# Optimization experiments

Measured on AMD Instinct MI355X. Metric: run time of the kernel, lower is better.

The kernel has to match this reference:

```python
import jax, jax.numpy as jnp
import numpy as np

DIM = 384
HEADS = 6
HEAD_DIM = DIM // HEADS
MLP_DIM = int(DIM * 4.0)
EPS = 1e-5


def layer_norm(x, g, b):
    mu = jnp.mean(x, axis=-1, keepdims=True)
    var = jnp.mean(jnp.square(x - mu), axis=-1, keepdims=True)
    return (x - mu) * jax.lax.rsqrt(var + EPS) * g + b


def setup_inputs() -> dict:
    key = jax.random.key(0)
    ks = jax.random.split(key, 12)
    s = 0.02
    return {
        "x": jax.random.normal(ks[0], (8, 2048, DIM), dtype=jnp.float32),
        "ln1_g": jnp.ones((DIM,), jnp.float32),
        "ln1_b": jnp.zeros((DIM,), jnp.float32),
        "qkv_w": jax.random.normal(ks[1], (DIM, 3 * DIM), jnp.float32) * s,
        "qkv_b": jnp.zeros((3 * DIM,), jnp.float32),
        "proj_w": jax.random.normal(ks[2], (DIM, DIM), jnp.float32) * s,
        "proj_b": jnp.zeros((DIM,), jnp.float32),
        "ln2_g": jnp.ones((DIM,), jnp.float32),
        "ln2_b": jnp.zeros((DIM,), jnp.float32),
        "fc1_w": jax.random.normal(ks[3], (DIM, MLP_DIM), jnp.float32) * s,
        "fc1_b": jnp.zeros((MLP_DIM,), jnp.float32),
        "fc2_w": jax.random.normal(ks[4], (MLP_DIM, DIM), jnp.float32) * s,
        "fc2_b": jnp.zeros((DIM,), jnp.float32),
    }


def reference(x, ln1_g, ln1_b, qkv_w, qkv_b, proj_w, proj_b,
              ln2_g, ln2_b, fc1_w, fc1_b, fc2_w, fc2_b):
    B, N, C = x.shape
    # --- attention ---
    h = layer_norm(x, ln1_g, ln1_b)
    qkv = h @ qkv_w + qkv_b  # [B,N,3C]
    qkv = qkv.reshape(B, N, 3, HEADS, HEAD_DIM)
    q, k, v = jnp.moveaxis(qkv, 2, 0)  # each [B,N,H,D]
    scale = HEAD_DIM ** -0.5
    attn = jnp.einsum('bnhd,bmhd->bhnm', q, k) * scale  # [B,H,N,N]
    attn = jax.nn.softmax(attn, axis=-1)
    o = jnp.einsum('bhnm,bmhd->bnhd', attn, v).reshape(B, N, C)
    x = x + o @ proj_w + proj_b
    # --- mlp ---
    h = layer_norm(x, ln2_g, ln2_b)
    h = jax.nn.gelu(h @ fc1_w + fc1_b, approximate=False)
    x = x + h @ fc2_w + fc2_b
    return x
```

## Files before the change

### kernel.cpp

```cpp
#include <hip/hip_runtime.h>
#include <hip/hip_bf16.h>

#define DIM   384
#define SEQ   2048
#define BATCH 8
#define NHEAD 6
#define HD    64
#define MLPD  1536
#define MTOT  (BATCH*SEQ)

typedef __attribute__((ext_vector_type(8))) short bf16x8;
typedef __attribute__((ext_vector_type(4))) float f32x4;

static __device__ __forceinline__ float bf2f(unsigned short u){
    union { float f; unsigned int i; } v; v.i = ((unsigned int)u) << 16; return v.f;
}
static __device__ __forceinline__ unsigned short f2bf(float f){
    union { float f; unsigned int i; } v; v.f = f;
    unsigned int r = v.i + 0x7fffu + ((v.i >> 16) & 1u);
    return (unsigned short)(r >> 16);
}
static __device__ __forceinline__ unsigned int asu(float f){
    union { float f; unsigned int i; } v; v.f = f; return v.i;
}
static __device__ __forceinline__ void gload_lds16(const unsigned short* g, unsigned short* l){
    __builtin_amdgcn_global_load_lds(
        (__attribute__((address_space(1))) void*)(g),
        (__attribute__((address_space(3))) void*)(l), 16, 0, 0);
}
static __device__ __forceinline__ void barx(){
    asm volatile("" ::: "memory");
    __builtin_amdgcn_s_barrier();
    asm volatile("" ::: "memory");
}
#define WAITVM(N) asm volatile("s_waitcnt vmcnt(" #N ")" ::: "memory")

static __device__ __forceinline__ int xcd_lin(){
    return (blockIdx.x & 7) * ((int)gridDim.x >> 3) + ((int)blockIdx.x >> 3);
}

__global__ __launch_bounds__(256) void wt_all_kernel(
    const float* __restrict__ qkv_w, const float* __restrict__ proj_w,
    const float* __restrict__ fc1_w, const float* __restrict__ fc2_w,
    unsigned short* __restrict__ o_qkv, unsigned short* __restrict__ o_prj,
    unsigned short* __restrict__ o_fc1, unsigned short* __restrict__ o_fc2)
{
    __shared__ float tile[64][68];
    int bid = blockIdx.x;
    const float* W; unsigned short* Wt; int K, N, tk, tn;
    if (bid < 108)      { W = qkv_w; Wt = o_qkv; K = 384;  N = 1152; tk = bid/18;        tn = bid%18; }
    else if (bid < 144) { W = proj_w; Wt = o_prj; K = 384;  N = 384;  tk = (bid-108)/6;  tn = (bid-108)%6; }
    else if (bid < 288) { W = fc1_w; Wt = o_fc1; K = 384;  N = 1536; tk = (bid-144)/24; tn = (bid-144)%24; }
    else                { W = fc2_w; Wt = o_fc2; K = 1536; N = 384;  tk = (bid-288)/6;  tn = (bid-288)%6; }
    int t = threadIdx.x;
    int lr = t >> 4, lc = (t & 15) * 4;
#pragma unroll
    for (int p = 0; p < 4; p++){
        float4 v = *(const float4*)(W + (size_t)(tk*64 + p*16 + lr) * N + tn*64 + lc);
        *(float4*)&tile[p*16 + lr][lc] = v;
    }
    __syncthreads();
    int n = t >> 2, k0 = (t & 3) * 16;
    unsigned int w[8];
#pragma unroll
    for (int i = 0; i < 8; i++)
        w[i] = (unsigned int)f2bf(tile[k0 + 2*i][n]) | ((unsigned int)f2bf(tile[k0 + 2*i + 1][n]) << 16);
    unsigned short* dst = Wt + (size_t)(tn*64 + n) * K + tk*64 + k0;
    *(uint4*)(dst)     = make_uint4(w[0], w[1], w[2], w[3]);
    *(uint4*)(dst + 8) = make_uint4(w[4], w[5], w[6], w[7]);
}

__global__ __launch_bounds__(256) void ln_kernel(const float* __restrict__ x,
                                                 const float* __restrict__ g,
                                                 const float* __restrict__ b,
                                                 unsigned short* __restrict__ out){
    int row  = blockIdx.x * 4 + (threadIdx.x >> 6);
    int lane = threadIdx.x & 63;
    const float* xr = x + (size_t)row * DIM;
    float v[6];
#pragma unroll
    for (int p = 0; p < 3; p++){
        float2 t = *(const float2*)(xr + lane * 2 + p * 128);
        v[2*p] = t.x; v[2*p+1] = t.y;
    }
    float s = 0.f, sq = 0.f;
#pragma unroll
    for (int i = 0; i < 6; i++){ s += v[i]; sq += v[i] * v[i]; }
#pragma unroll
    for (int off = 1; off < 64; off <<= 1){
        s  += __shfl_xor(s, off);
        sq += __shfl_xor(sq, off);
    }
    float mu   = s * (1.0f / DIM);
    float var  = sq * (1.0f / DIM) - mu * mu;
    float rstd = rsqrtf(var + 1e-5f);
    unsigned short* orow = out + (size_t)row * DIM;
#pragma unroll
    for (int p = 0; p < 3; p++){
        int c = lane * 2 + p * 128;
        float h0 = (v[2*p]   - mu) * rstd * g[c]   + b[c];
        float h1 = (v[2*p+1] - mu) * rstd * g[c+1] + b[c+1];
        unsigned int pk = (unsigned int)f2bf(h0) | ((unsigned int)f2bf(h1) << 16);
        *(unsigned int*)(orow + c) = pk;
    }
}

template<int EPI, int NC>
__global__ __launch_bounds__(128, 3) void gemm_kernel(
    const unsigned short* __restrict__ A, const unsigned short* __restrict__ Bt,
    const float* __restrict__ bias, int K, int N,
    const float* __restrict__ resid, float* __restrict__ outf,
    unsigned short* __restrict__ outb,
    unsigned short* __restrict__ qb, unsigned short* __restrict__ kb2,
    unsigned short* __restrict__ vb)
{
    __shared__ __align__(16) unsigned short smem[64*64 + 128*64];
    unsigned short* As = smem;
    unsigned short* Bs = smem + 64*64;
    int t = threadIdx.x;
    int wid = t >> 6, lane = t & 63, quad = lane >> 4, l15 = lane & 15;
    int lin = xcd_lin();
    int row0 = (lin / NC) * 64, col0 = (lin % NC) * 128;
    int sr = lane >> 3, sc = lane & 7;
    int scl = (sc ^ sr) * 8;

    const unsigned short* Ab = A  + (size_t)row0 * K;
    const unsigned short* Bb = Bt + (size_t)col0 * K;

    f32x4 acc[2][8];
    f32x4 zz = {0.f, 0.f, 0.f, 0.f};
#pragma unroll
    for (int i = 0; i < 2; i++)
#pragma unroll
        for (int j = 0; j < 8; j++) acc[i][j] = zz;

    for (int k0 = 0; k0 < K; k0 += 64){
        __syncthreads();
#pragma unroll
        for (int jj = 0; jj < 4; jj++){
            int rb = wid * 32 + jj * 8;
            gload_lds16(Ab + (size_t)(rb + sr) * K + k0 + scl, &As[rb * 64]);
        }
#pragma unroll
        for (int jj = 0; jj < 8; jj++){
            int rb = wid * 64 + jj * 8;
            gload_lds16(Bb + (size_t)(rb + sr) * K + k0 + scl, &Bs[rb * 64]);
        }
        __syncthreads();
#pragma unroll
        for (int kk = 0; kk < 2; kk++){
            bf16x8 af[2], bf[8];
#pragma unroll
            for (int i = 0; i < 2; i++){
                int r = wid*32 + i*16 + l15;
                af[i] = *(const bf16x8*)&As[r * 64 + (((kk*4 + quad) ^ (l15 & 7)) * 8)];
            }
#pragma unroll
            for (int j = 0; j < 8; j++){
                int r = j*16 + l15;
                bf[j] = *(const bf16x8*)&Bs[r * 64 + (((kk*4 + quad) ^ (l15 & 7)) * 8)];
            }
#pragma unroll
            for (int i = 0; i < 2; i++)
#pragma unroll
                for (int j = 0; j < 8; j++)
                    acc[i][j] = __builtin_amdgcn_mfma_f32_16x16x32_bf16(af[i], bf[j], acc[i][j], 0, 0, 0);
        }
    }

    if (EPI == 0 && col0 >= 768){
        __syncthreads();
        unsigned short* T = smem;
#pragma unroll
        for (int i = 0; i < 2; i++)
#pragma unroll
            for (int j = 0; j < 8; j++){
                int gcl = j*16 + l15;
                float bia = bias[col0 + gcl];
                int nsl0 = wid*32 + i*16 + quad*4;
#pragma unroll
                for (int r = 0; r < 4; r++)
                    T[gcl * 72 + nsl0 + r] = f2bf(acc[i][j][r] + bia);
            }
        __syncthreads();
        int rem = (col0 - 768) + t;
        int head = rem >> 6, d = rem & 63;
        int bidx = row0 >> 11, ns0 = row0 & 2047;
        unsigned short* dst = vb + ((size_t)((bidx * NHEAD + head) * 64 + d)) * SEQ + ns0;
        const unsigned short* src = T + t * 72;
#pragma unroll
        for (int m = 0; m < 8; m++)
            *(uint4*)(dst + m*8) = *(const uint4*)(src + m*8);
        return;
    }

#pragma unroll
    for (int i = 0; i < 2; i++){
#pragma unroll
        for (int j = 0; j < 8; j++){
            int gr0 = row0 + wid*32 + i*16 + quad*4;
            int gc  = col0 + j*16 + l15;
            float bia = bias[gc];
#pragma unroll
            for (int r = 0; r < 4; r++){
                int gr = gr0 + r;
                float val = acc[i][j][r] + bia;
                if (EPI == 1){
                    outf[(size_t)gr * N + gc] = resid[(size_t)gr * N + gc] + val;
                } else if (EPI == 2){
                    float u = val * (1.0f + 0.044715f * val * val);
                    float e = __builtin_amdgcn_exp2f(u * 2.3025851f);
                    outb[(size_t)gr * N + gc] = f2bf(val * e / (e + 1.0f));
                } else {
                    int trip = gc / 384, remq = gc - trip * 384;
                    int head = remq >> 6, d = remq & 63;
                    int bidx = gr >> 11, ns = gr & 2047;
                    size_t off = ((size_t)(bidx * NHEAD + head) * SEQ + ns) * 64 + d;
                    unsigned short* dstp = (trip == 0) ? qb : kb2;
                    dstp[off] = f2bf(val);
                }
            }
        }
    }
}

template<int LOFF>
static __device__ __forceinline__ void attn_tile(
    const bf16x8 (&qf)[2][2], const bf16x8& ones,
    const unsigned short* const (&kf_ptr)[4][2],
    const unsigned short* const (&vf_ptr)[2][4],
    const unsigned short* const (&pf_ptr)[2][2],
    uint2* const (&pw_ptr)[2][4],
    f32x4 (&sacc)[2], f32x4 (&oacc)[2][4])
{
    const f32x4 zz = {0.f, 0.f, 0.f, 0.f};
    f32x4 st[2][4];
#pragma unroll
    for (int n = 0; n < 4; n++){
        bf16x8 kf0 = *(const bf16x8*)(kf_ptr[n][0] + LOFF);
        bf16x8 kf1 = *(const bf16x8*)(kf_ptr[n][1] + LOFF);
#pragma unroll
        for (int h = 0; h < 2; h++){
            f32x4 z = __builtin_amdgcn_mfma_f32_16x16x32_bf16(kf0, qf[h][0], zz, 0, 0, 0);
            st[h][n] = __builtin_amdgcn_mfma_f32_16x16x32_bf16(kf1, qf[h][1], z, 0, 0, 0);
        }
    }
#pragma unroll
    for (int h = 0; h < 2; h++){
#pragma unroll
        for (int n = 0; n < 4; n++){
            float p0 = __builtin_amdgcn_exp2f(st[h][n][0]);
            float p1 = __builtin_amdgcn_exp2f(st[h][n][1]);
            float p2 = __builtin_amdgcn_exp2f(st[h][n][2]);
            float p3 = __builtin_amdgcn_exp2f(st[h][n][3]);
            unsigned int w0 = __builtin_amdgcn_perm(asu(p1), asu(p0), 0x07060302u);
            unsigned int w1 = __builtin_amdgcn_perm(asu(p3), asu(p2), 0x07060302u);
            *pw_ptr[h][n] = make_uint2(w0, w1);
        }
    }
    asm volatile("s_waitcnt lgkmcnt(0)" ::: "memory");
#pragma unroll
    for (int c = 0; c < 2; c++){
        bf16x8 pf[2];
#pragma unroll
        for (int h = 0; h < 2; h++)
            pf[h] = *(const bf16x8*)pf_ptr[c][h];
        sacc[0] = __builtin_amdgcn_mfma_f32_16x16x32_bf16(ones, pf[0], sacc[0], 0, 0, 0);
        sacc[1] = __builtin_amdgcn_mfma_f32_16x16x32_bf16(ones, pf[1], sacc[1], 0, 0, 0);
#pragma unroll
        for (int dn = 0; dn < 4; dn++){
            bf16x8 vf = *(const bf16x8*)(vf_ptr[c][dn] + LOFF);
            oacc[0][dn] = __builtin_amdgcn_mfma_f32_16x16x32_bf16(vf, pf[0], oacc[0][dn], 0, 0, 0);
            oacc[1][dn] = __builtin_amdgcn_mfma_f32_16x16x32_bf16(vf, pf[1], oacc[1][dn], 0, 0, 0);
        }
    }
}

__global__ __launch_bounds__(256, 3) void attn_kernel(const unsigned short* __restrict__ Q,
                                                      const unsigned short* __restrict__ Kb,
                                                      const unsigned short* __restrict__ Vt,
                                                      unsigned short* __restrict__ O){
    __shared__ __align__(16) unsigned short smem[16384 + 4*2048];

    int lin = xcd_lin();
    int qt = lin & 15, bh = lin >> 4;
    int t = threadIdx.x, wid = t >> 6, lane = t & 63, quad = lane >> 4, l15 = lane & 15;
    int l7 = l15 & 7;
    int q0 = qt * 128 + wid * 32;
    const unsigned short* Qp = Q  + (size_t)bh * SEQ * 64;
    const unsigned short* Kp = Kb + (size_t)bh * SEQ * 64;
    const unsigned short* Vp = Vt + (size_t)bh * 64 * SEQ;
    int sr = lane >> 3, sc = lane & 7;
    int scl = (sc ^ sr) * 8;

    const float QSCALE = 0.125f * 1.44269504f;
    bf16x8 qf[2][2];
#pragma unroll
    for (int h = 0; h < 2; h++){
#pragma unroll
        for (int c = 0; c < 2; c++){
            union { uint4 u; unsigned short s[8]; } cv;
            cv.u = *(const uint4*)(Qp + (size_t)(q0 + h*16 + l15) * 64 + c * 32 + quad * 8);
            bf16x8 f;
#pragma unroll
            for (int j = 0; j < 8; j++) f[j] = (short)f2bf(bf2f(cv.s[j]) * QSCALE);
            qf[h][c] = f;
        }
    }

    bf16x8 ones;
#pragma unroll
    for (int j = 0; j < 8; j++) ones[j] = (short)0x3F80;

    f32x4 oacc[2][4], sacc[2];
    f32x4 zz = {0.f, 0.f, 0.f, 0.f};
#pragma unroll
    for (int h = 0; h < 2; h++){
        sacc[h] = zz;
#pragma unroll
        for (int dn = 0; dn < 4; dn++) oacc[h][dn] = zz;
    }
    unsigned short* P = &smem[16384 + wid * 2048];

    const unsigned short* kf_ptr[4][2];
#pragma unroll
    for (int n = 0; n < 4; n++){
        int kv = n * 16 + l15;
        kf_ptr[n][0] = &smem[kv * 64 + ((quad       ^ (kv & 7)) * 8)];
        kf_ptr[n][1] = &smem[kv * 64 + (((4 + quad) ^ (kv & 7)) * 8)];
    }
    const unsigned short* vf_ptr[2][4];
#pragma unroll
    for (int c = 0; c < 2; c++)
#pragma unroll
        for (int dn = 0; dn < 4; dn++){
            int d = dn * 16 + l15;
            vf_ptr[c][dn] = &smem[4096 + d * 64 + (((c*4 + quad) ^ (d & 7)) * 8)];
        }
    const unsigned short* pf_ptr[2][2];
#pragma unroll
    for (int c = 0; c < 2; c++)
#pragma unroll
        for (int h = 0; h < 2; h++)
            pf_ptr[c][h] = P + (h*16 + l15) * 64 + (((c*4 + quad) ^ l7) * 8);
    uint2* pw_ptr[2][4];
#pragma unroll
    for (int h = 0; h < 2; h++)
#pragma unroll
        for (int n = 0; n < 4; n++){
            int qloc = h * 16 + l15;
            int chunk = n * 2 + (quad >> 1);
            pw_ptr[h][n] = (uint2*)(P + qloc * 64 + ((chunk ^ l7) * 8) + (quad & 1) * 4);
        }
    const unsigned short* kstage[2];
    const unsigned short* vstage[2];
    unsigned short* klds[2];
    unsigned short* vlds[2];
#pragma unroll
    for (int jj = 0; jj < 2; jj++){
        int rb = wid * 16 + jj * 8;
        kstage[jj] = Kp + (size_t)(rb + sr) * 64 + scl;
        vstage[jj] = Vp + (size_t)(rb + sr) * SEQ + scl;
        klds[jj] = &smem[rb * 64];
        vlds[jj] = &smem[4096 + rb * 64];
    }

#define AISSUE(BOFF) do { \
    _Pragma("unroll") \
    for (int jj = 0; jj < 2; jj++){ \
        gload_lds16(kstage[jj], klds[jj] + (BOFF)); \
        gload_lds16(vstage[jj], vlds[jj] + (BOFF)); \
        kstage[jj] += 64 * 64; \
        vstage[jj] += 64; \
    } } while(0)

    AISSUE(0);
    for (int p = 0; p < SEQ/128 - 1; p++){
        AISSUE(8192);
        WAITVM(4);
        barx();
        attn_tile<0>(qf, ones, kf_ptr, vf_ptr, pf_ptr, pw_ptr, sacc, oacc);
        barx();
        AISSUE(0);
        WAITVM(4);
        barx();
        attn_tile<8192>(qf, ones, kf_ptr, vf_ptr, pf_ptr, pw_ptr, sacc, oacc);
        barx();
    }
    AISSUE(8192);
    WAITVM(4);
    barx();
    attn_tile<0>(qf, ones, kf_ptr, vf_ptr, pf_ptr, pw_ptr, sacc, oacc);
    barx();
    WAITVM(0);
    barx();
    attn_tile<8192>(qf, ones, kf_ptr, vf_ptr, pf_ptr, pw_ptr, sacc, oacc);
#undef AISSUE

    int b = bh / NHEAD, hh = bh - b * NHEAD;
#pragma unroll
    for (int h = 0; h < 2; h++){
        float rd = 1.0f / sacc[h][0];
        size_t row = (size_t)(b * SEQ + q0 + h*16 + l15);
#pragma unroll
        for (int dn = 0; dn < 4; dn++){
            float v0 = oacc[h][dn][0] * rd, v1 = oacc[h][dn][1] * rd;
            float v2 = oacc[h][dn][2] * rd, v3 = oacc[h][dn][3] * rd;
            unsigned int w0 = (unsigned int)f2bf(v0) | ((unsigned int)f2bf(v1) << 16);
            unsigned int w1 = (unsigned int)f2bf(v2) | ((unsigned int)f2bf(v3) << 16);
            *(uint2*)(O + row * DIM + hh * 64 + dn * 16 + quad * 4) = make_uint2(w0, w1);
        }
    }
}

extern "C" void kernel_launch(void* const* d_in, const int* in_sizes, int n_in,
                              void* d_out, int out_size, void* d_ws, size_t ws_size,
                              hipStream_t stream){
    const float* x      = (const float*)d_in[0];
    const float* ln1_g  = (const float*)d_in[1];
    const float* ln1_b  = (const float*)d_in[2];
    const float* qkv_w  = (const float*)d_in[3];
    const float* qkv_b  = (const float*)d_in[4];
    const float* proj_w = (const float*)d_in[5];
    const float* proj_b = (const float*)d_in[6];
    const float* ln2_g  = (const float*)d_in[7];
    const float* ln2_b  = (const float*)d_in[8];
    const float* fc1_w  = (const float*)d_in[9];
    const float* fc1_b  = (const float*)d_in[10];
    const float* fc2_w  = (const float*)d_in[11];
    const float* fc2_b  = (const float*)d_in[12];
    float* out = (float*)d_out;

    char* p = (char*)d_ws;
    auto take = [&](size_t n){ char* r = p; p += (n + 255) & ~(size_t)255; return r; };
    unsigned short* wt_qkv = (unsigned short*)take((size_t)1152 * 384 * 2);
    unsigned short* wt_prj = (unsigned short*)take((size_t)384 * 384 * 2);
    unsigned short* wt_fc1 = (unsigned short*)take((size_t)1536 * 384 * 2);
    unsigned short* wt_fc2 = (unsigned short*)take((size_t)384 * 1536 * 2);
    unsigned short* rbig   = (unsigned short*)take((size_t)MTOT * 4 * DIM * 2);
    unsigned short* h2     = (unsigned short*)take((size_t)MTOT * DIM * 2);
    float*          x1     = (float*)take((size_t)MTOT * DIM * 4);

    unsigned short* h1     = rbig;
    unsigned short* qb     = rbig + (size_t)MTOT * DIM;
    unsigned short* kb     = qb   + (size_t)MTOT * DIM;
    unsigned short* vb     = kb   + (size_t)MTOT * DIM;
    unsigned short* attn_o = rbig;
    unsigned short* hm     = rbig;

    wt_all_kernel<<<dim3(432), 256, 0, stream>>>(qkv_w, proj_w, fc1_w, fc2_w,
                                                 wt_qkv, wt_prj, wt_fc1, wt_fc2);
    ln_kernel<<<dim3(MTOT/4), 256, 0, stream>>>(x, ln1_g, ln1_b, h1);
    gemm_kernel<0,9><<<dim3(2304), 128, 0, stream>>>(h1, wt_qkv, qkv_b, 384, 1152,
                                                     nullptr, nullptr, nullptr, qb, kb, vb);
    attn_kernel<<<dim3(768), 256, 0, stream>>>(qb, kb, vb, attn_o);
    gemm_kernel<1,3><<<dim3(768), 128, 0, stream>>>(attn_o, wt_prj, proj_b, 384, 384,
                                                    x, x1, nullptr, nullptr, nullptr, nullptr);
    ln_kernel<<<dim3(MTOT/4), 256, 0, stream>>>(x1, ln2_g, ln2_b, h2);
    gemm_kernel<2,12><<<dim3(3072), 128, 0, stream>>>(h2, wt_fc1, fc1_b, 384, 1536,
                                                      nullptr, nullptr, hm, nullptr, nullptr, nullptr);
    gemm_kernel<1,3><<<dim3(768), 128, 0, stream>>>(hm, wt_fc2, fc2_b, 1536, 384,
                                                    x1, out, nullptr, nullptr, nullptr, nullptr);
}
```

Measured before the change: 268.9 us.

## Enlarge GEMM tiles to 128x128 with 4 waves; add setprio around attention MFMAs

The GEMM kernel moves from 64x128 tiles with 2 waves to 128x128 tiles with 4 waves. Each wave still computes 32x128, and the B tile loaded into LDS is now shared by twice as many rows, which roughly halves B traffic per output. The V-transpose epilogue is split into two head halves so its staging buffer fits the new LDS layout, and grid sizes are halved to match. B fragments are now loaded and consumed one at a time, which lowers register pressure. Separately, the attention tile raises wave priority during its MFMA phases to help interleave with the exp work of other waves.

```diff
diff --git a/kernel.cpp b/kernel.cpp
--- a/kernel.cpp
+++ b/kernel.cpp
@@ -106,7 +106,7 @@
 }
 
 template<int EPI, int NC>
-__global__ __launch_bounds__(128, 3) void gemm_kernel(
+__global__ __launch_bounds__(256, 4) void gemm_kernel(
     const unsigned short* __restrict__ A, const unsigned short* __restrict__ Bt,
     const float* __restrict__ bias, int K, int N,
     const float* __restrict__ resid, float* __restrict__ outf,
@@ -114,13 +114,13 @@
     unsigned short* __restrict__ qb, unsigned short* __restrict__ kb2,
     unsigned short* __restrict__ vb)
 {
-    __shared__ __align__(16) unsigned short smem[64*64 + 128*64];
+    __shared__ __align__(16) unsigned short smem[2 * 8192];
     unsigned short* As = smem;
-    unsigned short* Bs = smem + 64*64;
+    unsigned short* Bs = smem + 8192;
     int t = threadIdx.x;
     int wid = t >> 6, lane = t & 63, quad = lane >> 4, l15 = lane & 15;
     int lin = xcd_lin();
-    int row0 = (lin / NC) * 64, col0 = (lin % NC) * 128;
+    int row0 = (lin / NC) * 128, col0 = (lin % NC) * 128;
     int sr = lane >> 3, sc = lane & 7;
     int scl = (sc ^ sr) * 8;
 
@@ -142,14 +142,14 @@
             gload_lds16(Ab + (size_t)(rb + sr) * K + k0 + scl, &As[rb * 64]);
         }
 #pragma unroll
-        for (int jj = 0; jj < 8; jj++){
-            int rb = wid * 64 + jj * 8;
+        for (int jj = 0; jj < 4; jj++){
+            int rb = wid * 32 + jj * 8;
             gload_lds16(Bb + (size_t)(rb + sr) * K + k0 + scl, &Bs[rb * 64]);
         }
         __syncthreads();
 #pragma unroll
         for (int kk = 0; kk < 2; kk++){
-            bf16x8 af[2], bf[8];
+            bf16x8 af[2];
 #pragma unroll
             for (int i = 0; i < 2; i++){
                 int r = wid*32 + i*16 + l15;
@@ -158,39 +158,40 @@
 #pragma unroll
             for (int j = 0; j < 8; j++){
                 int r = j*16 + l15;
-                bf[j] = *(const bf16x8*)&Bs[r * 64 + (((kk*4 + quad) ^ (l15 & 7)) * 8)];
+                bf16x8 bf = *(const bf16x8*)&Bs[r * 64 + (((kk*4 + quad) ^ (l15 & 7)) * 8)];
+                acc[0][j] = __builtin_amdgcn_mfma_f32_16x16x32_bf16(af[0], bf, acc[0][j], 0, 0, 0);
+                acc[1][j] = __builtin_amdgcn_mfma_f32_16x16x32_bf16(af[1], bf, acc[1][j], 0, 0, 0);
             }
+        }
+    }
+
+    if (EPI == 0 && col0 >= 768){
+        int bidx = row0 >> 11, ns0 = row0 & 2047;
+#pragma unroll
+        for (int half = 0; half < 2; half++){
+            __syncthreads();
+            unsigned short* T = smem;
 #pragma unroll
             for (int i = 0; i < 2; i++)
 #pragma unroll
-                for (int j = 0; j < 8; j++)
-                    acc[i][j] = __builtin_amdgcn_mfma_f32_16x16x32_bf16(af[i], bf[j], acc[i][j], 0, 0, 0);
-        }
-    }
-
-    if (EPI == 0 && col0 >= 768){
-        __syncthreads();
-        unsigned short* T = smem;
-#pragma unroll
-        for (int i = 0; i < 2; i++)
-#pragma unroll
-            for (int j = 0; j < 8; j++){
-                int gcl = j*16 + l15;
-                float bia = bias[col0 + gcl];
-                int nsl0 = wid*32 + i*16 + quad*4;
-#pragma unroll
-                for (int r = 0; r < 4; r++)
-                    T[gcl * 72 + nsl0 + r] = f2bf(acc[i][j][r] + bia);
-            }
-        __syncthreads();
-        int rem = (col0 - 768) + t;
-        int head = rem >> 6, d = rem & 63;
-        int bidx = row0 >> 11, ns0 = row0 & 2047;
-        unsigned short* dst = vb + ((size_t)((bidx * NHEAD + head) * 64 + d)) * SEQ + ns0;
-        const unsigned short* src = T + t * 72;
-#pragma unroll
-        for (int m = 0; m < 8; m++)
-            *(uint4*)(dst + m*8) = *(const uint4*)(src + m*8);
+                for (int jh = 0; jh < 4; jh++){
+                    int j = half*4 + jh;
+                    int d = jh*16 + l15;
+                    float bia = bias[col0 + half*64 + d];
+                    int nsl0 = wid*32 + i*16 + quad*4;
+#pragma unroll
+                    for (int r = 0; r < 4; r++)
+                        T[d * 136 + nsl0 + r] = f2bf(acc[i][j][r] + bia);
+                }
+            __syncthreads();
+            int head = ((col0 - 768) >> 6) + half;
+            int d = t >> 2, qq = t & 3;
+            unsigned short* dst = vb + ((size_t)((bidx * NHEAD + head) * 64 + d)) * SEQ + ns0 + qq*32;
+            const unsigned short* src = T + d * 136 + qq * 32;
+#pragma unroll
+            for (int m = 0; m < 4; m++)
+                *(uint4*)(dst + m*8) = *(const uint4*)(src + m*8);
+        }
         return;
     }
 
@@ -235,6 +236,7 @@
 {
     const f32x4 zz = {0.f, 0.f, 0.f, 0.f};
     f32x4 st[2][4];
+    __builtin_amdgcn_s_setprio(1);
 #pragma unroll
     for (int n = 0; n < 4; n++){
         bf16x8 kf0 = *(const bf16x8*)(kf_ptr[n][0] + LOFF);
@@ -245,6 +247,7 @@
             st[h][n] = __builtin_amdgcn_mfma_f32_16x16x32_bf16(kf1, qf[h][1], z, 0, 0, 0);
         }
     }
+    __builtin_amdgcn_s_setprio(0);
 #pragma unroll
     for (int h = 0; h < 2; h++){
 #pragma unroll
@@ -259,6 +262,7 @@
         }
     }
     asm volatile("s_waitcnt lgkmcnt(0)" ::: "memory");
+    __builtin_amdgcn_s_setprio(1);
 #pragma unroll
     for (int c = 0; c < 2; c++){
         bf16x8 pf[2];
@@ -274,6 +278,7 @@
             oacc[1][dn] = __builtin_amdgcn_mfma_f32_16x16x32_bf16(vf, pf[1], oacc[1][dn], 0, 0, 0);
         }
     }
+    __builtin_amdgcn_s_setprio(0);
 }
 
 __global__ __launch_bounds__(256, 3) void attn_kernel(const unsigned short* __restrict__ Q,
@@ -451,14 +456,14 @@
     wt_all_kernel<<<dim3(432), 256, 0, stream>>>(qkv_w, proj_w, fc1_w, fc2_w,
                                                  wt_qkv, wt_prj, wt_fc1, wt_fc2);
     ln_kernel<<<dim3(MTOT/4), 256, 0, stream>>>(x, ln1_g, ln1_b, h1);
-    gemm_kernel<0,9><<<dim3(2304), 128, 0, stream>>>(h1, wt_qkv, qkv_b, 384, 1152,
+    gemm_kernel<0,9><<<dim3(1152), 256, 0, stream>>>(h1, wt_qkv, qkv_b, 384, 1152,
                                                      nullptr, nullptr, nullptr, qb, kb, vb);
     attn_kernel<<<dim3(768), 256, 0, stream>>>(qb, kb, vb, attn_o);
-    gemm_kernel<1,3><<<dim3(768), 128, 0, stream>>>(attn_o, wt_prj, proj_b, 384, 384,
+    gemm_kernel<1,3><<<dim3(384), 256, 0, stream>>>(attn_o, wt_prj, proj_b, 384, 384,
                                                     x, x1, nullptr, nullptr, nullptr, nullptr);
     ln_kernel<<<dim3(MTOT/4), 256, 0, stream>>>(x1, ln2_g, ln2_b, h2);
-    gemm_kernel<2,12><<<dim3(3072), 128, 0, stream>>>(h2, wt_fc1, fc1_b, 384, 1536,
+    gemm_kernel<2,12><<<dim3(1536), 256, 0, stream>>>(h2, wt_fc1, fc1_b, 384, 1536,
                                                       nullptr, nullptr, hm, nullptr, nullptr, nullptr);
-    gemm_kernel<1,3><<<dim3(768), 128, 0, stream>>>(hm, wt_fc2, fc2_b, 1536, 384,
+    gemm_kernel<1,3><<<dim3(384), 256, 0, stream>>>(hm, wt_fc2, fc2_b, 1536, 384,
                                                     x1, out, nullptr, nullptr, nullptr, nullptr);
 }
```

After: 288.4 us. 7.3% more time.

## Add 32-row GEMM kernel for N=384 residual GEMMs and prioritize attention MFMA phases

Applied to the files above, without the earlier changes.

Adds a dedicated gemm32_kernel with 32x128 output tiles, used for the proj and fc2 GEMMs, whose output width of 384 left only 768 blocks with the old tile. The smaller row tile doubles the grid to 1536 blocks to fill more CUs, at the cost of more reloads of the B operand per output. The residual epilogue is removed from the generic GEMM. Separately, the attention tile raises wave priority with s_setprio around its MFMA phases, so that waves doing matrix work are favoured over those doing exp and LDS writes.

```diff
diff --git a/kernel.cpp b/kernel.cpp
--- a/kernel.cpp
+++ b/kernel.cpp
@@ -205,9 +205,7 @@
             for (int r = 0; r < 4; r++){
                 int gr = gr0 + r;
                 float val = acc[i][j][r] + bia;
-                if (EPI == 1){
-                    outf[(size_t)gr * N + gc] = resid[(size_t)gr * N + gc] + val;
-                } else if (EPI == 2){
+                if (EPI == 2){
                     float u = val * (1.0f + 0.044715f * val * val);
                     float e = __builtin_amdgcn_exp2f(u * 2.3025851f);
                     outb[(size_t)gr * N + gc] = f2bf(val * e / (e + 1.0f));
@@ -224,6 +222,82 @@
     }
 }
 
+template<int K>
+__global__ __launch_bounds__(128, 3) void gemm32_kernel(
+    const unsigned short* __restrict__ A, const unsigned short* __restrict__ Bt,
+    const float* __restrict__ bias, int N,
+    const float* __restrict__ resid, float* __restrict__ outf)
+{
+    __shared__ __align__(16) unsigned short smem[32*64 + 128*64];
+    unsigned short* As = smem;
+    unsigned short* Bs = smem + 32*64;
+    int t = threadIdx.x;
+    int wid = t >> 6, lane = t & 63, quad = lane >> 4, l15 = lane & 15;
+    int lin = xcd_lin();
+    int row0 = (lin / 3) * 32, col0 = (lin % 3) * 128;
+    int sr = lane >> 3, sc = lane & 7;
+    int scl = (sc ^ sr) * 8;
+
+    const unsigned short* Ab = A  + (size_t)row0 * K;
+    const unsigned short* Bb = Bt + (size_t)col0 * K;
+
+    f32x4 acc[2][4];
+    f32x4 zz = {0.f, 0.f, 0.f, 0.f};
+#pragma unroll
+    for (int i = 0; i < 2; i++)
+#pragma unroll
+        for (int j = 0; j < 4; j++) acc[i][j] = zz;
+
+    for (int k0 = 0; k0 < K; k0 += 64){
+        __syncthreads();
+#pragma unroll
+        for (int jj = 0; jj < 2; jj++){
+            int rb = wid * 16 + jj * 8;
+            gload_lds16(Ab + (size_t)(rb + sr) * K + k0 + scl, &As[rb * 64]);
+        }
+#pragma unroll
+        for (int jj = 0; jj < 8; jj++){
+            int rb = wid * 64 + jj * 8;
+            gload_lds16(Bb + (size_t)(rb + sr) * K + k0 + scl, &Bs[rb * 64]);
+        }
+        __syncthreads();
+#pragma unroll
+        for (int kk = 0; kk < 2; kk++){
+            bf16x8 af[2], bf[4];
+#pragma unroll
+            for (int i = 0; i < 2; i++){
+                int r = i*16 + l15;
+                af[i] = *(const bf16x8*)&As[r * 64 + (((kk*4 + quad) ^ (l15 & 7)) * 8)];
+            }
+#pragma unroll
+            for (int j = 0; j < 4; j++){
+                int r = wid*64 + j*16 + l15;
+                bf[j] = *(const bf16x8*)&Bs[r * 64 + (((kk*4 + quad) ^ (l15 & 7)) * 8)];
+            }
+#pragma unroll
+            for (int i = 0; i < 2; i++)
+#pragma unroll
+                for (int j = 0; j < 4; j++)
+                    acc[i][j] = __builtin_amdgcn_mfma_f32_16x16x32_bf16(af[i], bf[j], acc[i][j], 0, 0, 0);
+        }
+    }
+
+#pragma unroll
+    for (int i = 0; i < 2; i++){
+#pragma unroll
+        for (int j = 0; j < 4; j++){
+            int gr0 = row0 + i*16 + quad*4;
+            int gc  = col0 + wid*64 + j*16 + l15;
+            float bia = bias[gc];
+#pragma unroll
+            for (int r = 0; r < 4; r++){
+                int gr = gr0 + r;
+                outf[(size_t)gr * N + gc] = resid[(size_t)gr * N + gc] + acc[i][j][r] + bia;
+            }
+        }
+    }
+}
+
 template<int LOFF>
 static __device__ __forceinline__ void attn_tile(
     const bf16x8 (&qf)[2][2], const bf16x8& ones,
@@ -235,6 +309,7 @@
 {
     const f32x4 zz = {0.f, 0.f, 0.f, 0.f};
     f32x4 st[2][4];
+    __builtin_amdgcn_s_setprio(1);
 #pragma unroll
     for (int n = 0; n < 4; n++){
         bf16x8 kf0 = *(const bf16x8*)(kf_ptr[n][0] + LOFF);
@@ -245,6 +320,7 @@
             st[h][n] = __builtin_amdgcn_mfma_f32_16x16x32_bf16(kf1, qf[h][1], z, 0, 0, 0);
         }
     }
+    __builtin_amdgcn_s_setprio(0);
 #pragma unroll
     for (int h = 0; h < 2; h++){
 #pragma unroll
@@ -259,6 +335,7 @@
         }
     }
     asm volatile("s_waitcnt lgkmcnt(0)" ::: "memory");
+    __builtin_amdgcn_s_setprio(1);
 #pragma unroll
     for (int c = 0; c < 2; c++){
         bf16x8 pf[2];
@@ -274,6 +351,7 @@
             oacc[1][dn] = __builtin_amdgcn_mfma_f32_16x16x32_bf16(vf, pf[1], oacc[1][dn], 0, 0, 0);
         }
     }
+    __builtin_amdgcn_s_setprio(0);
 }
 
 __global__ __launch_bounds__(256, 3) void attn_kernel(const unsigned short* __restrict__ Q,
@@ -454,11 +532,11 @@
     gemm_kernel<0,9><<<dim3(2304), 128, 0, stream>>>(h1, wt_qkv, qkv_b, 384, 1152,
                                                      nullptr, nullptr, nullptr, qb, kb, vb);
     attn_kernel<<<dim3(768), 256, 0, stream>>>(qb, kb, vb, attn_o);
-    gemm_kernel<1,3><<<dim3(768), 128, 0, stream>>>(attn_o, wt_prj, proj_b, 384, 384,
-                                                    x, x1, nullptr, nullptr, nullptr, nullptr);
+    gemm32_kernel<384><<<dim3(1536), 128, 0, stream>>>(attn_o, wt_prj, proj_b, 384,
+                                                       x, x1);
     ln_kernel<<<dim3(MTOT/4), 256, 0, stream>>>(x1, ln2_g, ln2_b, h2);
     gemm_kernel<2,12><<<dim3(3072), 128, 0, stream>>>(h2, wt_fc1, fc1_b, 384, 1536,
                                                       nullptr, nullptr, hm, nullptr, nullptr, nullptr);
-    gemm_kernel<1,3><<<dim3(768), 128, 0, stream>>>(hm, wt_fc2, fc2_b, 1536, 384,
-                                                    x1, out, nullptr, nullptr, nullptr, nullptr);
-}
+    gemm32_kernel<1536><<<dim3(1536), 128, 0, stream>>>(hm, wt_fc2, fc2_b, 384,
+                                                        x1, out);
+}
```

Measured after the change: 285.4 us. 1.06x slower.
